# Performance work log

Measured on AMD Instinct MI355X. Metric: run time of the kernel, lower is better.

Reference implementation:

```python
import jax, jax.numpy as jnp
import numpy as np

B, C, OC, K, HW = 32, 256, 256, 3, 56
M, G = 2, 2
GAP = max(16, C // 16)          # input_gap = 16
MO = M * OC                      # fc1 out channels = 512
FC2_OUT = OC * C * K * K         # 589824
PER = FC2_OUT // MO              # per-group out channels of fc2 = 1152


def setup_inputs() -> dict:
    key = jax.random.key(0)
    ks = jax.random.split(key, 6)
    x = jax.random.normal(ks[0], (B, C, HW, HW), dtype=jnp.float32)
    reduce_w = jax.random.normal(ks[1], (GAP, C), dtype=jnp.float32) / np.sqrt(C)
    reduce_b = jnp.zeros((GAP,), dtype=jnp.float32)
    fc1_w = jax.random.normal(ks[2], (MO, GAP), dtype=jnp.float32) / np.sqrt(GAP)
    # fc2: grouped 1x1 conv, groups=G*OC=512, 1 in-channel per group -> weight (FC2_OUT,)
    fc2_w = jax.random.normal(ks[3], (FC2_OUT,), dtype=jnp.float32)
    fc2_b = jax.random.normal(ks[4], (FC2_OUT,), dtype=jnp.float32) * 0.01
    return {"x": x, "reduce_w": reduce_w, "reduce_b": reduce_b,
            "fc1_w": fc1_w, "fc2_w": fc2_w, "fc2_b": fc2_b}


def reference(x, reduce_w, reduce_b, fc1_w, fc2_w, fc2_b):
    b, c, h, w = x.shape
    # global average pool -> (b, C)
    gap = x.mean(axis=(2, 3))
    # reduce: 1x1 conv on 1x1 map == linear
    g = gap @ reduce_w.T + reduce_b                      # (b, GAP)
    # fc1 (no bias) + sigmoid
    a = jax.nn.sigmoid(g @ fc1_w.T)                      # (b, MO)
    # fc2: grouped 1x1 conv with 1 input channel per group:
    # out[:, g*PER + j] = a[:, g] * fc2_w[g*PER + j] + fc2_b[g*PER + j]
    wk = a[:, :, None] * fc2_w.reshape(MO, PER)[None] + fc2_b.reshape(MO, PER)[None]
    wk = wk.reshape(b * OC, c, K, K)                     # per-sample conv kernels
    pad = K // 2
    y = jax.lax.conv_general_dilated(
        x.reshape(1, b * c, h, w), wk,
        window_strides=(1, 1), padding=[(pad, pad), (pad, pad)],
        feature_group_count=b,
        dimension_numbers=("NCHW", "OIHW", "NCHW"))
    return y.reshape(b, OC, y.shape[2], y.shape[3])
```

## Files before the change

### kernel.cpp

```cpp
#include <hip/hip_runtime.h>
#include <hip/hip_bf16.h>
#include <stdint.h>

#define NB   32
#define NC   256
#define NOC  256
#define HWD  56
#define NPIX 3136
#define PW   58
#define PPIX 3364
#define KTOT 2304
#define MOD  512
#define GAPD 16

#define XBT_BYTES ((size_t)NB * PPIX * NC * 2)
#define WA_BYTES  ((size_t)NB * NOC * KTOT * 2)

typedef __bf16 bf16x8 __attribute__((ext_vector_type(8)));
typedef float  f32x4  __attribute__((ext_vector_type(4)));
typedef unsigned short u16x8 __attribute__((ext_vector_type(8)));

__device__ __forceinline__ unsigned short f2bf(float f) {
    union { float f; unsigned int u; } v; v.f = f;
    unsigned int u = v.u;
    return (unsigned short)((u + 0x7FFFu + ((u >> 16) & 1u)) >> 16);
}

__global__ void se_kernel(const float* __restrict__ gap,
                          const float* __restrict__ rw, const float* __restrict__ rb,
                          const float* __restrict__ f1w, float* __restrict__ a2) {
    __shared__ float sgap[NB * NC];
    __shared__ float sg[NB * GAPD];
    int t = threadIdx.x;
    #pragma unroll
    for (int i = 0; i < 16; ++i) sgap[i * 512 + t] = gap[i * 512 + t];
    __syncthreads();
    {
        int b = t >> 4, tt = t & 15;
        float s = rb[tt];
        for (int c = 0; c < NC; ++c) s += sgap[b * NC + c] * rw[tt * NC + c];
        sg[b * GAPD + tt] = s;
    }
    __syncthreads();
    for (int i = 0; i < 32; ++i) {
        int o = i * 512 + t;
        int b = o >> 9, m = o & 511;
        float s = 0.f;
        #pragma unroll
        for (int tt = 0; tt < GAPD; ++tt) s += sg[b * GAPD + tt] * f1w[m * GAPD + tt];
        a2[o] = 1.0f / (1.0f + __expf(-s));
    }
}

__global__ void wk_kernel(const float* __restrict__ a2,
                          const float* __restrict__ f2w, const float* __restrict__ f2b,
                          unsigned short* __restrict__ wa) {
    __shared__ float sw[KTOT];
    __shared__ float sbv[KTOT];
    __shared__ float sa[2 * NB];
    int oc = blockIdx.x, c = threadIdx.x;
    const float4* wsrc = (const float4*)(f2w + (size_t)oc * KTOT);
    const float4* bsrc = (const float4*)(f2b + (size_t)oc * KTOT);
    #pragma unroll
    for (int i = 0; i < 3; ++i) {
        int idx = i * 256 + c;
        if (idx < 576) {
            ((float4*)sw)[idx] = wsrc[idx];
            ((float4*)sbv)[idx] = bsrc[idx];
        }
    }
    if (c < 64) sa[c] = a2[(c >> 1) * MOD + 2 * oc + (c & 1)];
    __syncthreads();
    float w9[9], b9[9];
    #pragma unroll
    for (int s = 0; s < 9; ++s) { w9[s] = sw[c * 9 + s]; b9[s] = sbv[c * 9 + s]; }
    for (int b = 0; b < NB; ++b) {
        float a0 = sa[2 * b], a1 = sa[2 * b + 1];
        unsigned short* dst = wa + (size_t)(b * NOC + oc) * KTOT;
        #pragma unroll
        for (int s = 0; s < 9; ++s) {
            float a = ((c * 9 + s) >= 1152) ? a1 : a0;
            dst[s * NC + c] = f2bf(a * w9[s] + b9[s]);
        }
    }
}

__global__ void halo_kernel(unsigned short* __restrict__ xbt) {
    int b = blockIdx.x, t = threadIdx.x;
    unsigned short* xb = xbt + (size_t)b * PPIX * NC;
    u16x8 z = {};
    for (int i = t; i < 3712; i += 256) {
        int r = (i >= 1856) ? 1 : 0;
        int c = i - r * 1856;
        int pix = r * (57 * 58) + (c >> 5);
        *(u16x8*)(xb + (size_t)pix * NC + (c & 31) * 8) = z;
    }
    for (int i = t; i < 3584; i += 256) {
        int row = 1 + (i >> 6);
        int side = (i >> 5) & 1;
        int pix = row * PW + side * 57;
        *(u16x8*)(xb + (size_t)pix * NC + (i & 31) * 8) = z;
    }
}

#define TSTR 59
__global__ void xpose_kernel(const float* __restrict__ x, unsigned short* __restrict__ xbt,
                             float* __restrict__ gap) {
    __shared__ unsigned short tile[NC * TSTR];
    int py = blockIdx.x, b = blockIdx.y, t = threadIdx.x;
    int wv = t >> 6, l = t & 63;
    const float* xs = x + (size_t)b * NC * NPIX + py * HWD;
    int q = l & 15;
    int rb4 = l >> 4;
    #pragma unroll
    for (int it = 0; it < 16; ++it) {
        int c = wv * 64 + it * 4 + rb4;
        if (q < 14) {
            float4 v = *(const float4*)(xs + (size_t)c * NPIX + q * 4);
            unsigned short* tr = tile + c * TSTR + q * 4;
            tr[0] = f2bf(v.x); tr[1] = f2bf(v.y); tr[2] = f2bf(v.z); tr[3] = f2bf(v.w);
        }
    }
    __syncthreads();
    {
        float s = 0.f;
        #pragma unroll
        for (int px = 0; px < 56; ++px) {
            union { unsigned int u; float f; } cv;
            cv.u = ((unsigned int)tile[t * TSTR + px]) << 16;
            s += cv.f;
        }
        atomicAdd(&gap[b * NC + t], s * (1.0f / NPIX));
    }
    int cch = t & 31, pg = t >> 5;
    for (int i = 0; i < 7; ++i) {
        int px = pg * 7 + i;
        u16x8 v;
        #pragma unroll
        for (int j = 0; j < 8; ++j) v[j] = tile[(cch * 8 + j) * TSTR + px];
        *(u16x8*)(xbt + ((size_t)b * PPIX + (size_t)(1 + py) * PW + 1 + px) * NC + cch * 8) = v;
    }
}

#define SLICE 24576
#define BOFS  16384

__global__ __launch_bounds__(256, 2) void conv_gemm(
    const unsigned short* __restrict__ wa,
    const unsigned short* __restrict__ xbt,
    float* __restrict__ out)
{
    __shared__ __attribute__((aligned(16))) char lds[3 * SLICE];

    const int bid = blockIdx.x;
    const int wg  = (bid & 7) * 100 + (bid >> 3);
    const int b   = wg / 25, nt = wg % 25;

    const int t = threadIdx.x;
    const int w = t >> 6, l = t & 63;
    const int wm = w >> 1, wn = w & 1;

    const unsigned short* waB = wa + (size_t)b * NOC * KTOT;
    const unsigned short* xbB = xbt + (size_t)b * PPIX * NC;

    const int srow = l >> 2;
    const int sq8  = ((l & 3) ^ ((l >> 3) & 3)) * 8;
    const unsigned short* srcA[4];
    #pragma unroll
    for (int i = 0; i < 4; ++i) {
        int row = (i * 4 + w) * 16 + srow;
        srcA[i] = waB + (size_t)row * KTOT + sq8;
    }
    const unsigned short* srcB[2];
    #pragma unroll
    for (int i = 0; i < 2; ++i) {
        int row = (i * 4 + w) * 16 + srow;
        int pg = nt * 128 + row; if (pg > NPIX - 1) pg = NPIX - 1;
        int py = pg / 56, px = pg - py * 56;
        srcB[i] = xbB + (size_t)((py + 1) * PW + (px + 1)) * NC + sq8;
    }
    const int l16 = l * 16;

    auto issue = [&](int tp, int slot) {
        char* sb = lds + slot * SLICE;
        const int koff = tp * 32;
        const int s9 = tp >> 3;
        const int dy = (s9 >= 6) ? 2 : ((s9 >= 3) ? 1 : 0);
        const int dx = s9 - dy * 3;
        const int bsh = ((dy - 1) * PW + (dx - 1)) * NC + (tp & 7) * 32;
        #pragma unroll
        for (int i = 0; i < 4; ++i)
            __builtin_amdgcn_global_load_lds(
                (const __attribute__((address_space(1))) void*)(srcA[i] + koff),
                (__attribute__((address_space(3))) void*)(sb + (i * 4 + w) * 1024 + l16), 16, 0, 0);
        #pragma unroll
        for (int i = 0; i < 2; ++i)
            __builtin_amdgcn_global_load_lds(
                (const __attribute__((address_space(1))) void*)(srcB[i] + bsh),
                (__attribute__((address_space(3))) void*)(sb + BOFS + (i * 4 + w) * 1024 + l16), 16, 0, 0);
    };

    const int physq16 = (((l >> 4) ^ ((l >> 1) & 3)) << 4);
    const int arow = (l & 15) << 6;

    f32x4 acc[8][4] = {};

    auto compute = [&](int slot) {
        const char* sb = lds + slot * SLICE;
        bf16x8 af[8], bfr[4];
        #pragma unroll
        for (int i = 0; i < 8; ++i)
            af[i] = *(const bf16x8*)(sb + (wm * 8 + i) * 1024 + arow + physq16);
        #pragma unroll
        for (int j = 0; j < 4; ++j)
            bfr[j] = *(const bf16x8*)(sb + BOFS + (wn * 4 + j) * 1024 + arow + physq16);
        __builtin_amdgcn_s_setprio(1);
        #pragma unroll
        for (int i = 0; i < 8; ++i)
            #pragma unroll
            for (int j = 0; j < 4; ++j)
                acc[i][j] = __builtin_amdgcn_mfma_f32_16x16x32_bf16(af[i], bfr[j], acc[i][j], 0, 0, 0);
        __builtin_amdgcn_s_setprio(0);
    };

    issue(0, 0); issue(1, 1);

    int cs = 0;
    for (int p = 0; p < 70; ++p) {
        asm volatile("s_waitcnt vmcnt(6)" ::: "memory");
        __builtin_amdgcn_s_barrier();
        __builtin_amdgcn_sched_barrier(0);
        compute(cs);
        int ns = cs + 2; if (ns >= 3) ns -= 3;
        issue(p + 2, ns);
        ++cs; if (cs == 3) cs = 0;
    }
    asm volatile("s_waitcnt vmcnt(6)" ::: "memory");
    __builtin_amdgcn_s_barrier();
    __builtin_amdgcn_sched_barrier(0);
    compute(cs);
    ++cs; if (cs == 3) cs = 0;
    asm volatile("s_waitcnt vmcnt(0)" ::: "memory");
    __builtin_amdgcn_s_barrier();
    __builtin_amdgcn_sched_barrier(0);
    compute(cs);

    const int ocb = wm * 128 + ((l >> 4) << 2);
    const int pxb = nt * 128 + wn * 64 + (l & 15);
    #pragma unroll
    for (int i = 0; i < 8; ++i) {
        #pragma unroll
        for (int j = 0; j < 4; ++j) {
            int p = pxb + j * 16;
            if (p < NPIX) {
                float* o = out + ((size_t)(b * NOC + ocb + i * 16)) * NPIX + p;
                o[0]        = acc[i][j][0];
                o[NPIX]     = acc[i][j][1];
                o[2 * NPIX] = acc[i][j][2];
                o[3 * NPIX] = acc[i][j][3];
            }
        }
    }
}

extern "C" void kernel_launch(void* const* d_in, const int* in_sizes, int n_in,
                              void* d_out, int out_size, void* d_ws, size_t ws_size,
                              hipStream_t stream) {
    (void)in_sizes; (void)n_in; (void)out_size; (void)ws_size;
    const float* x   = (const float*)d_in[0];
    const float* rw  = (const float*)d_in[1];
    const float* rb  = (const float*)d_in[2];
    const float* f1w = (const float*)d_in[3];
    const float* f2w = (const float*)d_in[4];
    const float* f2b = (const float*)d_in[5];
    float* out = (float*)d_out;

    char* wsb = (char*)d_ws;
    unsigned short* xbt = (unsigned short*)wsb;
    unsigned short* wa  = (unsigned short*)(wsb + XBT_BYTES);
    float* gap = (float*)(wsb + XBT_BYTES + WA_BYTES);
    float* a2  = (float*)(wsb + XBT_BYTES + WA_BYTES + (size_t)NB * NC * 4);

    hipMemsetAsync(gap, 0, (size_t)NB * NC * 4, stream);
    halo_kernel<<<dim3(32), 256, 0, stream>>>(xbt);
    xpose_kernel<<<dim3(56, 32), 256, 0, stream>>>(x, xbt, gap);
    se_kernel<<<dim3(1), 512, 0, stream>>>(gap, rw, rb, f1w, a2);
    wk_kernel<<<dim3(256), 256, 0, stream>>>(a2, f2w, f2b, wa);
    conv_gemm<<<dim3(800), 256, 0, stream>>>(wa, xbt, out);
}
```

Before: 210.1 us.

## Retile conv GEMM to 128x224 tiles with A fragments loaded directly to registers

Changes the conv GEMM tile from 256 output channels x 128 pixels to 128 channels x 224 pixels, so 3136 pixels divide exactly into 14 tiles and the tail padding and bounds check go away. The weight (A) operand now skips LDS and is loaded straight from global memory into registers, while only the activation (B) operand is staged through a 4-slot LDS ring with a two-stage prefetch. This removes wasted MFMA work on padded pixels and frees LDS, but raises grid size to 896 blocks and makes A loads uncoalesced per-lane global reads whose latency must be hidden across phases.

```diff
diff --git a/kernel.cpp b/kernel.cpp
--- a/kernel.cpp
+++ b/kernel.cpp
@@ -142,125 +142,124 @@
     }
 }
 
-#define SLICE 24576
-#define BOFS  16384
 
 __global__ __launch_bounds__(256, 2) void conv_gemm(
     const unsigned short* __restrict__ wa,
     const unsigned short* __restrict__ xbt,
     float* __restrict__ out)
 {
-    __shared__ __attribute__((aligned(16))) char lds[3 * SLICE];
+    __shared__ __attribute__((aligned(16))) char lds[4 * 16384];
 
     const int bid = blockIdx.x;
-    const int wg  = (bid & 7) * 100 + (bid >> 3);
-    const int b   = wg / 25, nt = wg % 25;
+    const int wg  = (bid & 7) * 112 + (bid >> 3);
+    const int b   = wg / 28;
+    const int r28 = wg % 28;
+    const int oh  = r28 / 14, nt = r28 % 14;
 
     const int t = threadIdx.x;
     const int w = t >> 6, l = t & 63;
     const int wm = w >> 1, wn = w & 1;
 
-    const unsigned short* waB = wa + (size_t)b * NOC * KTOT;
+    const unsigned short* pA[4];
+    #pragma unroll
+    for (int m = 0; m < 4; ++m) {
+        int row = oh * 128 + wm * 64 + m * 16 + (l & 15);
+        pA[m] = wa + (size_t)(b * NOC + row) * KTOT + (l >> 4) * 8;
+    }
+
     const unsigned short* xbB = xbt + (size_t)b * PPIX * NC;
-
-    const int srow = l >> 2;
-    const int sq8  = ((l & 3) ^ ((l >> 3) & 3)) * 8;
-    const unsigned short* srcA[4];
-    #pragma unroll
-    for (int i = 0; i < 4; ++i) {
-        int row = (i * 4 + w) * 16 + srow;
-        srcA[i] = waB + (size_t)row * KTOT + sq8;
-    }
-    const unsigned short* srcB[2];
-    #pragma unroll
-    for (int i = 0; i < 2; ++i) {
-        int row = (i * 4 + w) * 16 + srow;
-        int pg = nt * 128 + row; if (pg > NPIX - 1) pg = NPIX - 1;
+    const unsigned short* pB[4];
+    #pragma unroll
+    for (int j = 0; j < 4; ++j) {
+        int s = j * 256 + t;
+        int row = s >> 2;
+        int q = (s & 3) ^ ((s >> 3) & 3);
+        int pg = nt * 224 + row;
         int py = pg / 56, px = pg - py * 56;
-        srcB[i] = xbB + (size_t)((py + 1) * PW + (px + 1)) * NC + sq8;
-    }
-    const int l16 = l * 16;
-
-    auto issue = [&](int tp, int slot) {
-        char* sb = lds + slot * SLICE;
-        const int koff = tp * 32;
-        const int s9 = tp >> 3;
-        const int dy = (s9 >= 6) ? 2 : ((s9 >= 3) ? 1 : 0);
-        const int dx = s9 - dy * 3;
-        const int bsh = ((dy - 1) * PW + (dx - 1)) * NC + (tp & 7) * 32;
-        #pragma unroll
-        for (int i = 0; i < 4; ++i)
-            __builtin_amdgcn_global_load_lds(
-                (const __attribute__((address_space(1))) void*)(srcA[i] + koff),
-                (__attribute__((address_space(3))) void*)(sb + (i * 4 + w) * 1024 + l16), 16, 0, 0);
-        #pragma unroll
-        for (int i = 0; i < 2; ++i)
-            __builtin_amdgcn_global_load_lds(
-                (const __attribute__((address_space(1))) void*)(srcB[i] + bsh),
-                (__attribute__((address_space(3))) void*)(sb + BOFS + (i * 4 + w) * 1024 + l16), 16, 0, 0);
-    };
+        pB[j] = xbB + (size_t)((py + 1) * PW + (px + 1)) * NC + q * 8;
+    }
 
     const int physq16 = (((l >> 4) ^ ((l >> 1) & 3)) << 4);
     const int arow = (l & 15) << 6;
 
-    f32x4 acc[8][4] = {};
-
-    auto compute = [&](int slot) {
-        const char* sb = lds + slot * SLICE;
-        bf16x8 af[8], bfr[4];
-        #pragma unroll
-        for (int i = 0; i < 8; ++i)
-            af[i] = *(const bf16x8*)(sb + (wm * 8 + i) * 1024 + arow + physq16);
-        #pragma unroll
-        for (int j = 0; j < 4; ++j)
-            bfr[j] = *(const bf16x8*)(sb + BOFS + (wn * 4 + j) * 1024 + arow + physq16);
-        __builtin_amdgcn_s_setprio(1);
-        #pragma unroll
-        for (int i = 0; i < 8; ++i)
-            #pragma unroll
-            for (int j = 0; j < 4; ++j)
-                acc[i][j] = __builtin_amdgcn_mfma_f32_16x16x32_bf16(af[i], bfr[j], acc[i][j], 0, 0, 0);
-        __builtin_amdgcn_s_setprio(0);
-    };
-
-    issue(0, 0); issue(1, 1);
-
-    int cs = 0;
-    for (int p = 0; p < 70; ++p) {
-        asm volatile("s_waitcnt vmcnt(6)" ::: "memory");
-        __builtin_amdgcn_s_barrier();
-        __builtin_amdgcn_sched_barrier(0);
-        compute(cs);
-        int ns = cs + 2; if (ns >= 3) ns -= 3;
-        issue(p + 2, ns);
-        ++cs; if (cs == 3) cs = 0;
-    }
-    asm volatile("s_waitcnt vmcnt(6)" ::: "memory");
-    __builtin_amdgcn_s_barrier();
-    __builtin_amdgcn_sched_barrier(0);
-    compute(cs);
-    ++cs; if (cs == 3) cs = 0;
-    asm volatile("s_waitcnt vmcnt(0)" ::: "memory");
-    __builtin_amdgcn_s_barrier();
-    __builtin_amdgcn_sched_barrier(0);
-    compute(cs);
-
-    const int ocb = wm * 128 + ((l >> 4) << 2);
-    const int pxb = nt * 128 + wn * 64 + (l & 15);
-    #pragma unroll
-    for (int i = 0; i < 8; ++i) {
-        #pragma unroll
-        for (int j = 0; j < 4; ++j) {
-            int p = pxb + j * 16;
-            if (p < NPIX) {
-                float* o = out + ((size_t)(b * NOC + ocb + i * 16)) * NPIX + p;
-                o[0]        = acc[i][j][0];
-                o[NPIX]     = acc[i][j][1];
-                o[2 * NPIX] = acc[i][j][2];
-                o[3 * NPIX] = acc[i][j][3];
-            }
-        }
-    }
+    f32x4 acc[4][7] = {};
+    bf16x8 aA[4], aB[4];
+
+#define STAGE_B(KT)                                                              \
+    do {                                                                         \
+        const int kn_ = (KT);                                                    \
+        const int s9_ = kn_ >> 3;                                                \
+        const int dy_ = (s9_ >= 6) ? 2 : ((s9_ >= 3) ? 1 : 0);                   \
+        const int dx_ = s9_ - dy_ * 3;                                           \
+        const int bsh_ = ((dy_ - 1) * PW + (dx_ - 1)) * NC + (kn_ & 7) * 32;     \
+        char* sb_ = lds + (kn_ & 3) * 16384;                                     \
+        _Pragma("unroll")                                                        \
+        for (int j = 0; j < 4; ++j)                                              \
+            __builtin_amdgcn_global_load_lds(                                    \
+                (const __attribute__((address_space(1))) void*)(pB[j] + bsh_),   \
+                (__attribute__((address_space(3))) void*)(sb_ + j * 4096 + w * 1024), \
+                16, 0, 0);                                                       \
+    } while (0)
+
+#define LOAD_A(KT, ASET)                                                         \
+    do {                                                                         \
+        _Pragma("unroll")                                                        \
+        for (int m = 0; m < 4; ++m)                                              \
+            ASET[m] = *(const bf16x8*)(pA[m] + (KT) * 32);                       \
+    } while (0)
+
+#define PHASE(P, ASET, DO_ISSUE, VM)                                             \
+    do {                                                                         \
+        asm volatile("s_waitcnt vmcnt(" VM ")" ::: "memory");                    \
+        __builtin_amdgcn_s_barrier();                                            \
+        __builtin_amdgcn_sched_barrier(0);                                       \
+        if (DO_ISSUE) STAGE_B((P) + 2);                                          \
+        const char* rb_ = lds + ((P) & 3) * 16384;                               \
+        bf16x8 bfr_[7];                                                          \
+        _Pragma("unroll")                                                        \
+        for (int nf = 0; nf < 7; ++nf)                                           \
+            bfr_[nf] = *(const bf16x8*)(rb_ + (wn * 7 + nf) * 1024 + arow + physq16); \
+        asm volatile("s_waitcnt lgkmcnt(0)" ::: "memory");                       \
+        __builtin_amdgcn_sched_barrier(0);                                       \
+        __builtin_amdgcn_s_setprio(1);                                           \
+        _Pragma("unroll")                                                        \
+        for (int m = 0; m < 4; ++m)                                              \
+            _Pragma("unroll")                                                    \
+            for (int nf = 0; nf < 7; ++nf)                                       \
+                acc[m][nf] = __builtin_amdgcn_mfma_f32_16x16x32_bf16(            \
+                    ASET[m], bfr_[nf], acc[m][nf], 0, 0, 0);                     \
+        __builtin_amdgcn_s_setprio(0);                                           \
+        if (DO_ISSUE) LOAD_A((P) + 2, ASET);                                     \
+    } while (0)
+
+    STAGE_B(0); LOAD_A(0, aA);
+    STAGE_B(1); LOAD_A(1, aB);
+
+    PHASE(0, aA, 1, "0");
+    PHASE(1, aB, 1, "8");
+    for (int p = 2; p < 70; p += 2) {
+        PHASE(p, aA, 1, "8");
+        PHASE(p + 1, aB, 1, "8");
+    }
+    PHASE(70, aA, 0, "8");
+    PHASE(71, aB, 0, "0");
+
+    const int ocb = oh * 128 + wm * 64 + ((l >> 4) << 2);
+    const int pxb = nt * 224 + wn * 112 + (l & 15);
+    #pragma unroll
+    for (int i = 0; i < 4; ++i) {
+        #pragma unroll
+        for (int j = 0; j < 7; ++j) {
+            float* o = out + ((size_t)(b * NOC + ocb + i * 16)) * NPIX + pxb + j * 16;
+            o[0]        = acc[i][j][0];
+            o[NPIX]     = acc[i][j][1];
+            o[2 * NPIX] = acc[i][j][2];
+            o[3 * NPIX] = acc[i][j][3];
+        }
+    }
+#undef PHASE
+#undef LOAD_A
+#undef STAGE_B
 }
 
 extern "C" void kernel_launch(void* const* d_in, const int* in_sizes, int n_in,
@@ -286,5 +285,5 @@
     xpose_kernel<<<dim3(56, 32), 256, 0, stream>>>(x, xbt, gap);
     se_kernel<<<dim3(1), 512, 0, stream>>>(gap, rw, rb, f1w, a2);
     wk_kernel<<<dim3(256), 256, 0, stream>>>(a2, f2w, f2b, wa);
-    conv_gemm<<<dim3(800), 256, 0, stream>>>(wa, xbt, out);
-}
+    conv_gemm<<<dim3(896), 256, 0, stream>>>(wa, xbt, out);
+}
```

New measurement: 279.0 us. 1.33x slower.

## Enlarge conv GEMM tile to 256x256 with 512 threads and phased K pipeline

Applied to the files above, without the earlier changes.

Doubles the pixel dimension of the per-block GEMM tile (256 output channels by 256 pixels), uses 8 waves per block and a K step of 64 with double-buffered LDS. Each K step is split into four phases so that A/B fragment reads, staging of the next half-tile via global_load_lds, and MFMA issue interleave. The goal is more reuse of the weight tile and fewer redundant loads. The cost is 128KB of LDS per block, which limits occupancy to one block per CU. It also brings more padding waste in the last pixel tile and a coarser grid of 416 blocks, which may leave a tail imbalance.

```diff
diff --git a/kernel.cpp b/kernel.cpp
--- a/kernel.cpp
+++ b/kernel.cpp
@@ -142,111 +142,121 @@
     }
 }
 
-#define SLICE 24576
-#define BOFS  16384
-
-__global__ __launch_bounds__(256, 2) void conv_gemm(
+
+#define AS1 __attribute__((address_space(1)))
+#define AS3 __attribute__((address_space(3)))
+
+__global__ __launch_bounds__(512, 2) void conv_gemm(
     const unsigned short* __restrict__ wa,
     const unsigned short* __restrict__ xbt,
     float* __restrict__ out)
 {
-    __shared__ __attribute__((aligned(16))) char lds[3 * SLICE];
+    __shared__ __attribute__((aligned(16))) char lds[131072];
 
     const int bid = blockIdx.x;
-    const int wg  = (bid & 7) * 100 + (bid >> 3);
-    const int b   = wg / 25, nt = wg % 25;
+    const int wg  = (bid & 7) * 52 + (bid >> 3);
+    const int nt  = wg % 13, b = wg / 13;
 
     const int t = threadIdx.x;
     const int w = t >> 6, l = t & 63;
-    const int wm = w >> 1, wn = w & 1;
+    const int wm = w >> 2, wn = w & 3;
 
     const unsigned short* waB = wa + (size_t)b * NOC * KTOT;
     const unsigned short* xbB = xbt + (size_t)b * PPIX * NC;
 
-    const int srow = l >> 2;
-    const int sq8  = ((l & 3) ^ ((l >> 3) & 3)) * 8;
-    const unsigned short* srcA[4];
-    #pragma unroll
-    for (int i = 0; i < 4; ++i) {
-        int row = (i * 4 + w) * 16 + srow;
-        srcA[i] = waB + (size_t)row * KTOT + sq8;
-    }
-    const unsigned short* srcB[2];
-    #pragma unroll
-    for (int i = 0; i < 2; ++i) {
-        int row = (i * 4 + w) * 16 + srow;
-        int pg = nt * 128 + row; if (pg > NPIX - 1) pg = NPIX - 1;
+    const unsigned short* pAs[2];
+    const unsigned short* pBs[2];
+    #pragma unroll
+    for (int j = 0; j < 2; ++j) {
+        int c = j * 512 + t;
+        int row = c >> 2;
+        int q = (c & 3) ^ ((c >> 3) & 3);
+        pAs[j] = waB + (size_t)row * KTOT + q * 8;
+        int pg = nt * 256 + row; if (pg > NPIX - 1) pg = NPIX - 1;
         int py = pg / 56, px = pg - py * 56;
-        srcB[i] = xbB + (size_t)((py + 1) * PW + (px + 1)) * NC + sq8;
-    }
-    const int l16 = l * 16;
-
-    auto issue = [&](int tp, int slot) {
-        char* sb = lds + slot * SLICE;
-        const int koff = tp * 32;
-        const int s9 = tp >> 3;
+        pBs[j] = xbB + (size_t)((py + 1) * PW + (px + 1)) * NC + q * 8;
+    }
+    const int t16 = t * 16;
+
+    auto stageA = [&](int kt, int kh) {
+        char* dst = lds + (kt & 1) * 65536 + kh * 16384;
+        #pragma unroll
+        for (int j = 0; j < 2; ++j)
+            __builtin_amdgcn_global_load_lds(
+                (const AS1 void*)(pAs[j] + kt * 64 + kh * 32),
+                (AS3 void*)(dst + j * 8192 + t16), 16, 0, 0);
+    };
+    auto stageB = [&](int kt, int kh) {
+        char* dst = lds + (kt & 1) * 65536 + 32768 + kh * 16384;
+        const int s9 = kt >> 2;
         const int dy = (s9 >= 6) ? 2 : ((s9 >= 3) ? 1 : 0);
         const int dx = s9 - dy * 3;
-        const int bsh = ((dy - 1) * PW + (dx - 1)) * NC + (tp & 7) * 32;
-        #pragma unroll
-        for (int i = 0; i < 4; ++i)
+        const int off = ((dy - 1) * PW + (dx - 1)) * NC + (kt & 3) * 64 + kh * 32;
+        #pragma unroll
+        for (int j = 0; j < 2; ++j)
             __builtin_amdgcn_global_load_lds(
-                (const __attribute__((address_space(1))) void*)(srcA[i] + koff),
-                (__attribute__((address_space(3))) void*)(sb + (i * 4 + w) * 1024 + l16), 16, 0, 0);
-        #pragma unroll
-        for (int i = 0; i < 2; ++i)
-            __builtin_amdgcn_global_load_lds(
-                (const __attribute__((address_space(1))) void*)(srcB[i] + bsh),
-                (__attribute__((address_space(3))) void*)(sb + BOFS + (i * 4 + w) * 1024 + l16), 16, 0, 0);
+                (const AS1 void*)(pBs[j] + off),
+                (AS3 void*)(dst + j * 8192 + t16), 16, 0, 0);
     };
 
-    const int physq16 = (((l >> 4) ^ ((l >> 1) & 3)) << 4);
-    const int arow = (l & 15) << 6;
+    const int laneRow = (l & 15) * 64;
+    const int laneQ   = (((l >> 4) ^ ((l >> 1) & 3)) << 4);
 
     f32x4 acc[8][4] = {};
-
-    auto compute = [&](int slot) {
-        const char* sb = lds + slot * SLICE;
-        bf16x8 af[8], bfr[4];
-        #pragma unroll
-        for (int i = 0; i < 8; ++i)
-            af[i] = *(const bf16x8*)(sb + (wm * 8 + i) * 1024 + arow + physq16);
-        #pragma unroll
-        for (int j = 0; j < 4; ++j)
-            bfr[j] = *(const bf16x8*)(sb + BOFS + (wn * 4 + j) * 1024 + arow + physq16);
-        __builtin_amdgcn_s_setprio(1);
-        #pragma unroll
-        for (int i = 0; i < 8; ++i)
-            #pragma unroll
-            for (int j = 0; j < 4; ++j)
-                acc[i][j] = __builtin_amdgcn_mfma_f32_16x16x32_bf16(af[i], bfr[j], acc[i][j], 0, 0, 0);
-        __builtin_amdgcn_s_setprio(0);
-    };
-
-    issue(0, 0); issue(1, 1);
-
-    int cs = 0;
-    for (int p = 0; p < 70; ++p) {
-        asm volatile("s_waitcnt vmcnt(6)" ::: "memory");
-        __builtin_amdgcn_s_barrier();
-        __builtin_amdgcn_sched_barrier(0);
-        compute(cs);
-        int ns = cs + 2; if (ns >= 3) ns -= 3;
-        issue(p + 2, ns);
-        ++cs; if (cs == 3) cs = 0;
-    }
-    asm volatile("s_waitcnt vmcnt(6)" ::: "memory");
-    __builtin_amdgcn_s_barrier();
-    __builtin_amdgcn_sched_barrier(0);
-    compute(cs);
-    ++cs; if (cs == 3) cs = 0;
-    asm volatile("s_waitcnt vmcnt(0)" ::: "memory");
-    __builtin_amdgcn_s_barrier();
-    __builtin_amdgcn_sched_barrier(0);
-    compute(cs);
+    bf16x8 bfr[4];
+
+#define VM8  asm volatile("s_waitcnt vmcnt(8)" ::: "memory")
+#define VM4  asm volatile("s_waitcnt vmcnt(4)" ::: "memory")
+#define VM0  asm volatile("s_waitcnt vmcnt(0)" ::: "memory")
+
+#define PHASE(MH, KH, DB, STAGE_STMT)                                             \
+    do {                                                                          \
+        __builtin_amdgcn_s_barrier();                                             \
+        __builtin_amdgcn_sched_barrier(0);                                        \
+        const char* ab_ = (DB) + (KH) * 16384;                                    \
+        bf16x8 af_[4];                                                            \
+        _Pragma("unroll")                                                         \
+        for (int m = 0; m < 4; ++m)                                               \
+            af_[m] = *(const bf16x8*)(ab_ + (wm * 8 + (MH) * 4 + m) * 1024        \
+                                      + laneRow + laneQ);                         \
+        if ((MH) == 0) {                                                          \
+            _Pragma("unroll")                                                     \
+            for (int n = 0; n < 4; ++n)                                           \
+                bfr[n] = *(const bf16x8*)(ab_ + 32768 + (wn * 4 + n) * 1024       \
+                                          + laneRow + laneQ);                     \
+        }                                                                         \
+        STAGE_STMT;                                                               \
+        __builtin_amdgcn_s_setprio(1);                                            \
+        _Pragma("unroll")                                                         \
+        for (int m = 0; m < 4; ++m)                                               \
+            _Pragma("unroll")                                                     \
+            for (int n = 0; n < 4; ++n)                                           \
+                acc[(MH) * 4 + m][n] = __builtin_amdgcn_mfma_f32_16x16x32_bf16(   \
+                    af_[m], bfr[n], acc[(MH) * 4 + m][n], 0, 0, 0);               \
+        __builtin_amdgcn_s_setprio(0);                                            \
+    } while (0)
+
+    stageA(0, 0); stageB(0, 0); stageA(0, 1); stageB(0, 1);
+    stageA(1, 0); stageB(1, 0);
+
+    for (int tt = 0; tt < 35; ++tt) {
+        char* dc = lds + (tt & 1) * 65536;
+        VM8; PHASE(0, 0, dc, { stageA(tt + 1, 1); });
+             PHASE(1, 0, dc, { stageB(tt + 1, 1); });
+        VM8; PHASE(0, 1, dc, { if (tt < 34) stageA(tt + 2, 0); });
+             PHASE(1, 1, dc, { if (tt < 34) stageB(tt + 2, 0); });
+    }
+    {
+        char* dc = lds + 65536;
+        VM4; PHASE(0, 0, dc, {});
+             PHASE(1, 0, dc, {});
+        VM0; PHASE(0, 1, dc, {});
+             PHASE(1, 1, dc, {});
+    }
+#undef PHASE
 
     const int ocb = wm * 128 + ((l >> 4) << 2);
-    const int pxb = nt * 128 + wn * 64 + (l & 15);
+    const int pxb = nt * 256 + wn * 64 + (l & 15);
     #pragma unroll
     for (int i = 0; i < 8; ++i) {
         #pragma unroll
@@ -286,5 +296,5 @@
     xpose_kernel<<<dim3(56, 32), 256, 0, stream>>>(x, xbt, gap);
     se_kernel<<<dim3(1), 512, 0, stream>>>(gap, rw, rb, f1w, a2);
     wk_kernel<<<dim3(256), 256, 0, stream>>>(a2, f2w, f2b, wa);
-    conv_gemm<<<dim3(800), 256, 0, stream>>>(wa, xbt, out);
-}
+    conv_gemm<<<dim3(416), 512, 0, stream>>>(wa, xbt, out);
+}
```

Result: no change. 206.7 us (-1.6%).
